# Kernel tuning notes

Measured on AMD Instinct MI355X. Metric: run time of the kernel, lower is better.

The kernel has to match this reference:

```python
import jax, jax.numpy as jnp
import numpy as np

N_NODES = 100000


def _gcn_conv(x, W, b, src, dst, ew, num_nodes):
    # PyG GCNConv: symmetric normalization with self-loops already included
    # in (src, dst, ew). deg computed on destination (col) index.
    deg = jax.ops.segment_sum(ew, dst, num_segments=num_nodes)  # [N]
    dinv = jnp.where(deg > 0, jax.lax.rsqrt(deg), 0.0)          # [N]
    norm = dinv[src] * ew * dinv[dst]                           # [E]
    h = x @ W                                                   # [N, out]
    msg = h[src] * norm[:, None]                                # [E, out] gather+scale
    out = jax.ops.segment_sum(msg, dst, num_segments=num_nodes) # scatter-add
    return out + b


def setup_inputs() -> dict:
    key = jax.random.key(0)
    k = jax.random.split(key, 8)
    in_c, hid_c, out_c = 128, 128, 64
    E, EL = 1600000, 200000
    x = jax.random.normal(k[0], (N_NODES, in_c), dtype=jnp.float32)
    edge_index = jax.random.randint(k[1], (2, E), 0, N_NODES, dtype=jnp.int64)
    edge_weight = jax.random.uniform(k[2], (E,), dtype=jnp.float32)
    edge_label_index = jax.random.randint(k[3], (2, EL), 0, N_NODES, dtype=jnp.int64)
    # Glorot-ish params
    W1 = jax.random.normal(k[4], (in_c, hid_c), dtype=jnp.float32) / np.sqrt(in_c)
    b1 = jnp.zeros((hid_c,), dtype=jnp.float32)
    W2 = jax.random.normal(k[5], (hid_c, out_c), dtype=jnp.float32) / np.sqrt(hid_c)
    b2 = jnp.zeros((out_c,), dtype=jnp.float32)
    return {"x": x, "edge_index": edge_index, "edge_weight": edge_weight,
            "edge_label_index": edge_label_index,
            "W1": W1, "b1": b1, "W2": W2, "b2": b2}


def reference(x, edge_index, edge_weight, edge_label_index, W1, b1, W2, b2):
    n = x.shape[0]
    # add self-loops (weight 1.0), static shape
    loop = jnp.arange(n, dtype=edge_index.dtype)
    src = jnp.concatenate([edge_index[0], loop])
    dst = jnp.concatenate([edge_index[1], loop])
    ew = jnp.concatenate([edge_weight, jnp.ones((n,), dtype=edge_weight.dtype)])
    h = jax.nn.relu(_gcn_conv(x, W1, b1, src, dst, ew, n))
    z = _gcn_conv(h, W2, b2, src, dst, ew, n)          # [N, out_c]
    # decode: edge dot-product
    return (z[edge_label_index[0]] * z[edge_label_index[1]]).sum(axis=-1)
```

## Files before the change

kernel.cpp:

```cpp
#include <hip/hip_runtime.h>
#include <math.h>

__global__ __launch_bounds__(256) void gemm128_hist_kernel(
        const float* __restrict__ X, const float* __restrict__ W, float* __restrict__ Y, int n,
        const int* __restrict__ dst, int* __restrict__ cnt, int* __restrict__ rank, int E) {
    constexpr int CG  = 32;
    constexpr int RG  = 8;
    constexpr int M   = 64;
    constexpr int RT  = 8;
    constexpr int KC  = 32;
    constexpr int LDX = 132;
    __shared__ float  Xl[M * LDX];
    __shared__ float4 Wl[KC * CG];

    const int bid = blockIdx.x;
    const int t = threadIdx.x;
    const int EPB = (E + (int)gridDim.x - 1) / (int)gridDim.x;
    const int eBeg = bid * EPB;
    const int eEnd = min(eBeg + EPB, E);

    if ((bid & 1) == 0) {
        for (int e = eBeg + t; e < eEnd; e += 256)
            rank[e] = atomicAdd(&cnt[dst[e]], 1);
    }

    int row0 = bid * M;
    {
        const float4* Xg = (const float4*)X;
        for (int f = t; f < M * 32; f += 256) {
            int r = f >> 5, c4 = f & 31;
            int gr = row0 + r;
            float4 v = make_float4(0.f, 0.f, 0.f, 0.f);
            if (gr < n) v = Xg[(size_t)gr * 32 + c4];
            *(float4*)&Xl[r * LDX + c4 * 4] = v;
        }
    }

    int cg = t % CG;
    int r0 = (t / CG) * RT;

    float4 acc[RT];
#pragma unroll
    for (int r = 0; r < RT; r++) acc[r] = make_float4(0.f, 0.f, 0.f, 0.f);

    const float4* Wg = (const float4*)W;
    for (int kc = 0; kc < 128; kc += KC) {
        __syncthreads();
        for (int f = t; f < KC * CG; f += 256)
            Wl[f] = Wg[(size_t)kc * CG + f];
        __syncthreads();
#pragma unroll 4
        for (int k = 0; k < KC; k += 4) {
            float4 b0 = Wl[(k + 0) * CG + cg];
            float4 b1 = Wl[(k + 1) * CG + cg];
            float4 b2 = Wl[(k + 2) * CG + cg];
            float4 b3 = Wl[(k + 3) * CG + cg];
#pragma unroll
            for (int r = 0; r < RT; r++) {
                float4 a = *(float4*)&Xl[(r0 + r) * LDX + kc + k];
                acc[r].x += a.x * b0.x + a.y * b1.x + a.z * b2.x + a.w * b3.x;
                acc[r].y += a.x * b0.y + a.y * b1.y + a.z * b2.y + a.w * b3.y;
                acc[r].z += a.x * b0.z + a.y * b1.z + a.z * b2.z + a.w * b3.z;
                acc[r].w += a.x * b0.w + a.y * b1.w + a.z * b2.w + a.w * b3.w;
            }
        }
    }

#pragma unroll
    for (int r = 0; r < RT; r++) {
        int gr = row0 + r0 + r;
        if (gr < n) *(float4*)&Y[(size_t)gr * 128 + cg * 4] = acc[r];
    }

    if (bid & 1) {
        for (int e = eBeg + t; e < eEnd; e += 256)
            rank[e] = atomicAdd(&cnt[dst[e]], 1);
    }
}

__global__ __launch_bounds__(256) void scan_block(const int* __restrict__ in, int* __restrict__ out,
                                                  int* __restrict__ bsum, int n) {
    __shared__ int s[256];
    int tid = threadIdx.x;
    int base = blockIdx.x * 1024 + tid * 4;
    int a0 = (base + 0 < n) ? in[base + 0] : 0;
    int a1 = (base + 1 < n) ? in[base + 1] : 0;
    int a2 = (base + 2 < n) ? in[base + 2] : 0;
    int a3 = (base + 3 < n) ? in[base + 3] : 0;
    int tsum = a0 + a1 + a2 + a3;
    s[tid] = tsum;
    __syncthreads();
    for (int off = 1; off < 256; off <<= 1) {
        int v = (tid >= off) ? s[tid - off] : 0;
        __syncthreads();
        s[tid] += v;
        __syncthreads();
    }
    int texcl = s[tid] - tsum;
    if (base + 0 < n) out[base + 0] = texcl;
    if (base + 1 < n) out[base + 1] = texcl + a0;
    if (base + 2 < n) out[base + 2] = texcl + a0 + a1;
    if (base + 3 < n) out[base + 3] = texcl + a0 + a1 + a2;
    if (tid == 255) bsum[blockIdx.x] = s[255];
}

__global__ __launch_bounds__(256) void scan_bsums(int* __restrict__ bsum, int nb) {
    __shared__ int s[256];
    __shared__ int carry_s;
    int tid = threadIdx.x;
    if (tid == 0) carry_s = 0;
    __syncthreads();
    for (int base = 0; base < nb; base += 256) {
        int v = (base + tid < nb) ? bsum[base + tid] : 0;
        int orig = v;
        s[tid] = v;
        __syncthreads();
        for (int off = 1; off < 256; off <<= 1) {
            int u = (tid >= off) ? s[tid - off] : 0;
            __syncthreads();
            s[tid] += u;
            __syncthreads();
        }
        int carry = carry_s;
        int excl = s[tid] - orig + carry;
        if (base + tid < nb) bsum[base + tid] = excl;
        int tot = s[255];
        __syncthreads();
        if (tid == 0) carry_s = carry + tot;
        __syncthreads();
    }
}

__global__ void scan_add(int* __restrict__ rowptr, const int* __restrict__ bscan, int n) {
    int t = blockIdx.x * blockDim.x + threadIdx.x;
    if (t < n) rowptr[t] += bscan[t >> 10];
}

__global__ void scatter_pairs(const int* __restrict__ src, const int* __restrict__ dst,
                              const float* __restrict__ ew, const int* __restrict__ rowptr,
                              const int* __restrict__ rank, int2* __restrict__ pairs, int E) {
    int e = blockIdx.x * blockDim.x + threadIdx.x;
    if (e >= E) return;
    int d = dst[e];
    int p = rowptr[d] + rank[e];
    pairs[p] = make_int2(src[e], __float_as_int(ew[e]));
}

__global__ void deg_dinv_kernel(const int2* __restrict__ pairs, const int* __restrict__ rowptr,
                                float* __restrict__ dinv, int n) {
    int i = blockIdx.x * blockDim.x + threadIdx.x;
    if (i >= n) return;
    int beg = rowptr[i], end = rowptr[i + 1];
    float s = 0.f;
    for (int j = beg; j < end; j++) s += __int_as_float(pairs[j].y);
    dinv[i] = 1.0f / sqrtf(s + 1.0f);
}

__global__ void norm_kernel(int2* __restrict__ pairs, const float* __restrict__ dinv, int E) {
    int j = blockIdx.x * blockDim.x + threadIdx.x;
    if (j >= E) return;
    int2 pr = pairs[j];
    pairs[j].y = __float_as_int(__int_as_float(pr.y) * dinv[pr.x]);
}

__global__ __launch_bounds__(256) void gather_mv_kernel(const float* __restrict__ H,
                                                        const int* __restrict__ rowptr,
                                                        const int2* __restrict__ pairs,
                                                        const float* __restrict__ dinv,
                                                        const float* __restrict__ bias,
                                                        const float* __restrict__ W2,
                                                        float* __restrict__ Z, int n) {
    __shared__ float h1s[8 * 128];
    __shared__ float w2s[32 * 64];
    const int t = threadIdx.x;
    const int nl = t >> 5;
    const int c4 = t & 31;
    const int node = blockIdx.x * 8 + nl;
    const float4* H4 = (const float4*)H;

    float4 a0 = make_float4(0.f, 0.f, 0.f, 0.f);
    float di = 0.f;
    if (node < n) {
        int beg = rowptr[node], end = rowptr[node + 1];
        di = dinv[node];
        float4 hv = H4[(size_t)node * 32 + c4];
        a0.x = hv.x * di; a0.y = hv.y * di; a0.z = hv.z * di; a0.w = hv.w * di;
        float4 a1 = make_float4(0.f, 0.f, 0.f, 0.f);
        float4 a2 = make_float4(0.f, 0.f, 0.f, 0.f);
        float4 a3 = make_float4(0.f, 0.f, 0.f, 0.f);
        int j = beg;
        for (; j + 8 <= end; j += 8) {
            int2 p0 = pairs[j + 0], p1 = pairs[j + 1], p2 = pairs[j + 2], p3 = pairs[j + 3];
            int2 p4 = pairs[j + 4], p5 = pairs[j + 5], p6 = pairs[j + 6], p7 = pairs[j + 7];
            float4 v0 = H4[(size_t)p0.x * 32 + c4];
            float4 v1 = H4[(size_t)p1.x * 32 + c4];
            float4 v2 = H4[(size_t)p2.x * 32 + c4];
            float4 v3 = H4[(size_t)p3.x * 32 + c4];
            float4 v4 = H4[(size_t)p4.x * 32 + c4];
            float4 v5 = H4[(size_t)p5.x * 32 + c4];
            float4 v6 = H4[(size_t)p6.x * 32 + c4];
            float4 v7 = H4[(size_t)p7.x * 32 + c4];
            float w0 = __int_as_float(p0.y), w1 = __int_as_float(p1.y);
            float w2 = __int_as_float(p2.y), w3 = __int_as_float(p3.y);
            float w4 = __int_as_float(p4.y), w5 = __int_as_float(p5.y);
            float w6 = __int_as_float(p6.y), w7 = __int_as_float(p7.y);
            a0.x += v0.x * w0; a0.y += v0.y * w0; a0.z += v0.z * w0; a0.w += v0.w * w0;
            a1.x += v1.x * w1; a1.y += v1.y * w1; a1.z += v1.z * w1; a1.w += v1.w * w1;
            a2.x += v2.x * w2; a2.y += v2.y * w2; a2.z += v2.z * w2; a2.w += v2.w * w2;
            a3.x += v3.x * w3; a3.y += v3.y * w3; a3.z += v3.z * w3; a3.w += v3.w * w3;
            a0.x += v4.x * w4; a0.y += v4.y * w4; a0.z += v4.z * w4; a0.w += v4.w * w4;
            a1.x += v5.x * w5; a1.y += v5.y * w5; a1.z += v5.z * w5; a1.w += v5.w * w5;
            a2.x += v6.x * w6; a2.y += v6.y * w6; a2.z += v6.z * w6; a2.w += v6.w * w6;
            a3.x += v7.x * w7; a3.y += v7.y * w7; a3.z += v7.z * w7; a3.w += v7.w * w7;
        }
        if (j + 4 <= end) {
            int2 p0 = pairs[j + 0], p1 = pairs[j + 1], p2 = pairs[j + 2], p3 = pairs[j + 3];
            float4 v0 = H4[(size_t)p0.x * 32 + c4];
            float4 v1 = H4[(size_t)p1.x * 32 + c4];
            float4 v2 = H4[(size_t)p2.x * 32 + c4];
            float4 v3 = H4[(size_t)p3.x * 32 + c4];
            float w0 = __int_as_float(p0.y), w1 = __int_as_float(p1.y);
            float w2 = __int_as_float(p2.y), w3 = __int_as_float(p3.y);
            a0.x += v0.x * w0; a0.y += v0.y * w0; a0.z += v0.z * w0; a0.w += v0.w * w0;
            a1.x += v1.x * w1; a1.y += v1.y * w1; a1.z += v1.z * w1; a1.w += v1.w * w1;
            a2.x += v2.x * w2; a2.y += v2.y * w2; a2.z += v2.z * w2; a2.w += v2.w * w2;
            a3.x += v3.x * w3; a3.y += v3.y * w3; a3.z += v3.z * w3; a3.w += v3.w * w3;
            j += 4;
        }
        for (; j < end; j++) {
            int2 pr = pairs[j];
            float w = __int_as_float(pr.y);
            float4 v = H4[(size_t)pr.x * 32 + c4];
            a0.x += v.x * w; a0.y += v.y * w; a0.z += v.z * w; a0.w += v.w * w;
        }
        float4 bb = ((const float4*)bias)[c4];
        a0.x = fmaxf(((a0.x + a1.x) + (a2.x + a3.x)) * di + bb.x, 0.f);
        a0.y = fmaxf(((a0.y + a1.y) + (a2.y + a3.y)) * di + bb.y, 0.f);
        a0.z = fmaxf(((a0.z + a1.z) + (a2.z + a3.z)) * di + bb.z, 0.f);
        a0.w = fmaxf(((a0.w + a1.w) + (a2.w + a3.w)) * di + bb.w, 0.f);
    }
    *(float4*)&h1s[nl * 128 + c4 * 4] = a0;

    float z0 = 0.f, z1 = 0.f;
    for (int kc = 0; kc < 128; kc += 32) {
        __syncthreads();
        {
            const float4* W2g = (const float4*)(W2 + kc * 64);
            float4* w2s4 = (float4*)w2s;
            for (int f = t; f < 512; f += 256) w2s4[f] = W2g[f];
        }
        __syncthreads();
        const float* hrow = &h1s[nl * 128 + kc];
        const float2* w2c = (const float2*)w2s;
#pragma unroll 8
        for (int k = 0; k < 32; k++) {
            float hk = hrow[k];
            float2 w = w2c[k * 32 + c4];
            z0 += hk * w.x;
            z1 += hk * w.y;
        }
    }
    if (node < n) *(float2*)&Z[(size_t)node * 64 + c4 * 2] = make_float2(z0, z1);
}

template<int C, bool RELU>
__global__ __launch_bounds__(256) void gather_reduce(const float* __restrict__ H,
                                                     const int* __restrict__ rowptr,
                                                     const int2* __restrict__ pairs,
                                                     const float* __restrict__ dinv,
                                                     const float* __restrict__ bias,
                                                     float* __restrict__ out, int n) {
    constexpr int TPN = C / 4;
    int t = blockIdx.x * blockDim.x + threadIdx.x;
    int node = t / TPN;
    int c4 = t % TPN;
    if (node >= n) return;
    const float4* H4 = (const float4*)H;
    int beg = rowptr[node], end = rowptr[node + 1];
    float di = dinv[node];
    float4 hv = H4[(size_t)node * TPN + c4];
    float4 bb = ((const float4*)bias)[c4];
    float4 a0, a1, a2, a3;
    a0.x = hv.x * di; a0.y = hv.y * di; a0.z = hv.z * di; a0.w = hv.w * di;
    a1 = make_float4(0.f, 0.f, 0.f, 0.f);
    a2 = make_float4(0.f, 0.f, 0.f, 0.f);
    a3 = make_float4(0.f, 0.f, 0.f, 0.f);
    int j = beg;
    for (; j + 8 <= end; j += 8) {
        int2 p0 = pairs[j + 0], p1 = pairs[j + 1], p2 = pairs[j + 2], p3 = pairs[j + 3];
        int2 p4 = pairs[j + 4], p5 = pairs[j + 5], p6 = pairs[j + 6], p7 = pairs[j + 7];
        float4 v0 = H4[(size_t)p0.x * TPN + c4];
        float4 v1 = H4[(size_t)p1.x * TPN + c4];
        float4 v2 = H4[(size_t)p2.x * TPN + c4];
        float4 v3 = H4[(size_t)p3.x * TPN + c4];
        float4 v4 = H4[(size_t)p4.x * TPN + c4];
        float4 v5 = H4[(size_t)p5.x * TPN + c4];
        float4 v6 = H4[(size_t)p6.x * TPN + c4];
        float4 v7 = H4[(size_t)p7.x * TPN + c4];
        float w0 = __int_as_float(p0.y), w1 = __int_as_float(p1.y);
        float w2 = __int_as_float(p2.y), w3 = __int_as_float(p3.y);
        float w4 = __int_as_float(p4.y), w5 = __int_as_float(p5.y);
        float w6 = __int_as_float(p6.y), w7 = __int_as_float(p7.y);
        a0.x += v0.x * w0; a0.y += v0.y * w0; a0.z += v0.z * w0; a0.w += v0.w * w0;
        a1.x += v1.x * w1; a1.y += v1.y * w1; a1.z += v1.z * w1; a1.w += v1.w * w1;
        a2.x += v2.x * w2; a2.y += v2.y * w2; a2.z += v2.z * w2; a2.w += v2.w * w2;
        a3.x += v3.x * w3; a3.y += v3.y * w3; a3.z += v3.z * w3; a3.w += v3.w * w3;
        a0.x += v4.x * w4; a0.y += v4.y * w4; a0.z += v4.z * w4; a0.w += v4.w * w4;
        a1.x += v5.x * w5; a1.y += v5.y * w5; a1.z += v5.z * w5; a1.w += v5.w * w5;
        a2.x += v6.x * w6; a2.y += v6.y * w6; a2.z += v6.z * w6; a2.w += v6.w * w6;
        a3.x += v7.x * w7; a3.y += v7.y * w7; a3.z += v7.z * w7; a3.w += v7.w * w7;
    }
    if (j + 4 <= end) {
        int2 p0 = pairs[j + 0], p1 = pairs[j + 1], p2 = pairs[j + 2], p3 = pairs[j + 3];
        float4 v0 = H4[(size_t)p0.x * TPN + c4];
        float4 v1 = H4[(size_t)p1.x * TPN + c4];
        float4 v2 = H4[(size_t)p2.x * TPN + c4];
        float4 v3 = H4[(size_t)p3.x * TPN + c4];
        float w0 = __int_as_float(p0.y), w1 = __int_as_float(p1.y);
        float w2 = __int_as_float(p2.y), w3 = __int_as_float(p3.y);
        a0.x += v0.x * w0; a0.y += v0.y * w0; a0.z += v0.z * w0; a0.w += v0.w * w0;
        a1.x += v1.x * w1; a1.y += v1.y * w1; a1.z += v1.z * w1; a1.w += v1.w * w1;
        a2.x += v2.x * w2; a2.y += v2.y * w2; a2.z += v2.z * w2; a2.w += v2.w * w2;
        a3.x += v3.x * w3; a3.y += v3.y * w3; a3.z += v3.z * w3; a3.w += v3.w * w3;
        j += 4;
    }
    for (; j < end; j++) {
        int2 pr = pairs[j];
        float w = __int_as_float(pr.y);
        float4 v = H4[(size_t)pr.x * TPN + c4];
        a0.x += v.x * w; a0.y += v.y * w; a0.z += v.z * w; a0.w += v.w * w;
    }
    float4 acc;
    acc.x = ((a0.x + a1.x) + (a2.x + a3.x)) * di + bb.x;
    acc.y = ((a0.y + a1.y) + (a2.y + a3.y)) * di + bb.y;
    acc.z = ((a0.z + a1.z) + (a2.z + a3.z)) * di + bb.z;
    acc.w = ((a0.w + a1.w) + (a2.w + a3.w)) * di + bb.w;
    if (RELU) {
        acc.x = fmaxf(acc.x, 0.f);
        acc.y = fmaxf(acc.y, 0.f);
        acc.z = fmaxf(acc.z, 0.f);
        acc.w = fmaxf(acc.w, 0.f);
    }
    *(float4*)&out[(size_t)node * C + c4 * 4] = acc;
}

__global__ void decode_kernel(const float* __restrict__ Z, const int* __restrict__ ea,
                              const int* __restrict__ eb, float* __restrict__ out, int L) {
    int t = blockIdx.x * blockDim.x + threadIdx.x;
    int e = t >> 4;
    int c = (t & 15) << 2;
    if (e >= L) return;
    float4 za = *(const float4*)&Z[(size_t)ea[e] * 64 + c];
    float4 zb = *(const float4*)&Z[(size_t)eb[e] * 64 + c];
    float p = za.x * zb.x + za.y * zb.y + za.z * zb.z + za.w * zb.w;
    p += __shfl_xor(p, 1);
    p += __shfl_xor(p, 2);
    p += __shfl_xor(p, 4);
    p += __shfl_xor(p, 8);
    if ((t & 15) == 0) out[e] = p;
}

extern "C" void kernel_launch(void* const* d_in, const int* in_sizes, int n_in,
                              void* d_out, int out_size, void* d_ws, size_t ws_size,
                              hipStream_t stream) {
    const float* x   = (const float*)d_in[0];
    const int*   ei  = (const int*)d_in[1];
    const float* ew  = (const float*)d_in[2];
    const int*   eli = (const int*)d_in[3];
    const float* W1  = (const float*)d_in[4];
    const float* b1  = (const float*)d_in[5];
    const float* W2  = (const float*)d_in[6];
    const float* b2  = (const float*)d_in[7];
    float* out = (float*)d_out;

    const int N = in_sizes[0] / 128;
    const int E = in_sizes[2];
    const int L = in_sizes[3] / 2;
    const int NP = ((N + 255) / 256) * 256;

    float* ws     = (float*)d_ws;
    float* dinv   = ws;
    int*   cnt    = (int*)(ws + NP);
    int*   rowptr = cnt + NP;
    int*   bsum   = rowptr + NP;
    int*   rank   = bsum + 1024;
    int2*  pairs  = (int2*)(rank + E);
    float* A      = (float*)(pairs + E);
    float* B      = A + (size_t)NP * 128;

    const int n1 = N + 1;
    const int nb = (n1 + 1023) / 1024;

    hipMemsetAsync(cnt, 0, (size_t)n1 * 4, stream);

    const int Gg = (N + 63) / 64;
    gemm128_hist_kernel<<<Gg, 256, 0, stream>>>(x, W1, A, N, ei + E, cnt, rank, E);

    scan_block<<<nb, 256, 0, stream>>>(cnt, rowptr, bsum, n1);
    scan_bsums<<<1, 256, 0, stream>>>(bsum, nb);
    scan_add<<<(n1 + 255) / 256, 256, 0, stream>>>(rowptr, bsum, n1);
    scatter_pairs<<<(E + 255) / 256, 256, 0, stream>>>(ei, ei + E, ew, rowptr, rank, pairs, E);
    deg_dinv_kernel<<<(N + 255) / 256, 256, 0, stream>>>(pairs, rowptr, dinv, N);
    norm_kernel<<<(E + 255) / 256, 256, 0, stream>>>(pairs, dinv, E);

    gather_mv_kernel<<<(N + 7) / 8, 256, 0, stream>>>(A, rowptr, pairs, dinv, b1, W2, B, N);

    gather_reduce<64, false><<<(N * 16 + 255) / 256, 256, 0, stream>>>(B, rowptr, pairs, dinv, b2, A, N);

    decode_kernel<<<(L * 16 + 255) / 256, 256, 0, stream>>>(A, eli, eli + L, out, L);
}
```

Baseline: 491.9 us.

## Fold source-side normalization into gather kernels and stage full W2 in LDS once

```diff
diff --git a/kernel.cpp b/kernel.cpp
--- a/kernel.cpp
+++ b/kernel.cpp
@@ -156,13 +156,6 @@
     dinv[i] = 1.0f / sqrtf(s + 1.0f);
 }
 
-__global__ void norm_kernel(int2* __restrict__ pairs, const float* __restrict__ dinv, int E) {
-    int j = blockIdx.x * blockDim.x + threadIdx.x;
-    if (j >= E) return;
-    int2 pr = pairs[j];
-    pairs[j].y = __float_as_int(__int_as_float(pr.y) * dinv[pr.x]);
-}
-
 __global__ __launch_bounds__(256) void gather_mv_kernel(const float* __restrict__ H,
                                                         const int* __restrict__ rowptr,
                                                         const int2* __restrict__ pairs,
@@ -171,18 +164,24 @@
                                                         const float* __restrict__ W2,
                                                         float* __restrict__ Z, int n) {
     __shared__ float h1s[8 * 128];
-    __shared__ float w2s[32 * 64];
+    __shared__ float w2s[128 * 64];
     const int t = threadIdx.x;
     const int nl = t >> 5;
     const int c4 = t & 31;
     const int node = blockIdx.x * 8 + nl;
     const float4* H4 = (const float4*)H;
 
+    {
+        const float4* W2g = (const float4*)W2;
+        float4* w2s4 = (float4*)w2s;
+#pragma unroll
+        for (int f = 0; f < 8; f++) w2s4[f * 256 + t] = W2g[f * 256 + t];
+    }
+
     float4 a0 = make_float4(0.f, 0.f, 0.f, 0.f);
-    float di = 0.f;
     if (node < n) {
         int beg = rowptr[node], end = rowptr[node + 1];
-        di = dinv[node];
+        float di = dinv[node];
         float4 hv = H4[(size_t)node * 32 + c4];
         a0.x = hv.x * di; a0.y = hv.y * di; a0.z = hv.z * di; a0.w = hv.w * di;
         float4 a1 = make_float4(0.f, 0.f, 0.f, 0.f);
@@ -200,10 +199,14 @@
             float4 v5 = H4[(size_t)p5.x * 32 + c4];
             float4 v6 = H4[(size_t)p6.x * 32 + c4];
             float4 v7 = H4[(size_t)p7.x * 32 + c4];
-            float w0 = __int_as_float(p0.y), w1 = __int_as_float(p1.y);
-            float w2 = __int_as_float(p2.y), w3 = __int_as_float(p3.y);
-            float w4 = __int_as_float(p4.y), w5 = __int_as_float(p5.y);
-            float w6 = __int_as_float(p6.y), w7 = __int_as_float(p7.y);
+            float w0 = dinv[p0.x] * __int_as_float(p0.y);
+            float w1 = dinv[p1.x] * __int_as_float(p1.y);
+            float w2 = dinv[p2.x] * __int_as_float(p2.y);
+            float w3 = dinv[p3.x] * __int_as_float(p3.y);
+            float w4 = dinv[p4.x] * __int_as_float(p4.y);
+            float w5 = dinv[p5.x] * __int_as_float(p5.y);
+            float w6 = dinv[p6.x] * __int_as_float(p6.y);
+            float w7 = dinv[p7.x] * __int_as_float(p7.y);
             a0.x += v0.x * w0; a0.y += v0.y * w0; a0.z += v0.z * w0; a0.w += v0.w * w0;
             a1.x += v1.x * w1; a1.y += v1.y * w1; a1.z += v1.z * w1; a1.w += v1.w * w1;
             a2.x += v2.x * w2; a2.y += v2.y * w2; a2.z += v2.z * w2; a2.w += v2.w * w2;
@@ -219,8 +222,10 @@
             float4 v1 = H4[(size_t)p1.x * 32 + c4];
             float4 v2 = H4[(size_t)p2.x * 32 + c4];
             float4 v3 = H4[(size_t)p3.x * 32 + c4];
-            float w0 = __int_as_float(p0.y), w1 = __int_as_float(p1.y);
-            float w2 = __int_as_float(p2.y), w3 = __int_as_float(p3.y);
+            float w0 = dinv[p0.x] * __int_as_float(p0.y);
+            float w1 = dinv[p1.x] * __int_as_float(p1.y);
+            float w2 = dinv[p2.x] * __int_as_float(p2.y);
+            float w3 = dinv[p3.x] * __int_as_float(p3.y);
             a0.x += v0.x * w0; a0.y += v0.y * w0; a0.z += v0.z * w0; a0.w += v0.w * w0;
             a1.x += v1.x * w1; a1.y += v1.y * w1; a1.z += v1.z * w1; a1.w += v1.w * w1;
             a2.x += v2.x * w2; a2.y += v2.y * w2; a2.z += v2.z * w2; a2.w += v2.w * w2;
@@ -229,7 +234,7 @@
         }
         for (; j < end; j++) {
             int2 pr = pairs[j];
-            float w = __int_as_float(pr.y);
+            float w = dinv[pr.x] * __int_as_float(pr.y);
             float4 v = H4[(size_t)pr.x * 32 + c4];
             a0.x += v.x * w; a0.y += v.y * w; a0.z += v.z * w; a0.w += v.w * w;
         }
@@ -240,25 +245,17 @@
         a0.w = fmaxf(((a0.w + a1.w) + (a2.w + a3.w)) * di + bb.w, 0.f);
     }
     *(float4*)&h1s[nl * 128 + c4 * 4] = a0;
+    __syncthreads();
 
     float z0 = 0.f, z1 = 0.f;
-    for (int kc = 0; kc < 128; kc += 32) {
-        __syncthreads();
-        {
-            const float4* W2g = (const float4*)(W2 + kc * 64);
-            float4* w2s4 = (float4*)w2s;
-            for (int f = t; f < 512; f += 256) w2s4[f] = W2g[f];
-        }
-        __syncthreads();
-        const float* hrow = &h1s[nl * 128 + kc];
-        const float2* w2c = (const float2*)w2s;
+    const float* hrow = &h1s[nl * 128];
+    const float2* w2c = (const float2*)w2s;
 #pragma unroll 8
-        for (int k = 0; k < 32; k++) {
-            float hk = hrow[k];
-            float2 w = w2c[k * 32 + c4];
-            z0 += hk * w.x;
-            z1 += hk * w.y;
-        }
+    for (int k = 0; k < 128; k++) {
+        float hk = hrow[k];
+        float2 w = w2c[k * 32 + c4];
+        z0 += hk * w.x;
+        z1 += hk * w.y;
     }
     if (node < n) *(float2*)&Z[(size_t)node * 64 + c4 * 2] = make_float2(z0, z1);
 }
@@ -297,10 +294,14 @@
         float4 v5 = H4[(size_t)p5.x * TPN + c4];
         float4 v6 = H4[(size_t)p6.x * TPN + c4];
         float4 v7 = H4[(size_t)p7.x * TPN + c4];
-        float w0 = __int_as_float(p0.y), w1 = __int_as_float(p1.y);
-        float w2 = __int_as_float(p2.y), w3 = __int_as_float(p3.y);
-        float w4 = __int_as_float(p4.y), w5 = __int_as_float(p5.y);
-        float w6 = __int_as_float(p6.y), w7 = __int_as_float(p7.y);
+        float w0 = dinv[p0.x] * __int_as_float(p0.y);
+        float w1 = dinv[p1.x] * __int_as_float(p1.y);
+        float w2 = dinv[p2.x] * __int_as_float(p2.y);
+        float w3 = dinv[p3.x] * __int_as_float(p3.y);
+        float w4 = dinv[p4.x] * __int_as_float(p4.y);
+        float w5 = dinv[p5.x] * __int_as_float(p5.y);
+        float w6 = dinv[p6.x] * __int_as_float(p6.y);
+        float w7 = dinv[p7.x] * __int_as_float(p7.y);
         a0.x += v0.x * w0; a0.y += v0.y * w0; a0.z += v0.z * w0; a0.w += v0.w * w0;
         a1.x += v1.x * w1; a1.y += v1.y * w1; a1.z += v1.z * w1; a1.w += v1.w * w1;
         a2.x += v2.x * w2; a2.y += v2.y * w2; a2.z += v2.z * w2; a2.w += v2.w * w2;
@@ -316,8 +317,10 @@
         float4 v1 = H4[(size_t)p1.x * TPN + c4];
         float4 v2 = H4[(size_t)p2.x * TPN + c4];
         float4 v3 = H4[(size_t)p3.x * TPN + c4];
-        float w0 = __int_as_float(p0.y), w1 = __int_as_float(p1.y);
-        float w2 = __int_as_float(p2.y), w3 = __int_as_float(p3.y);
+        float w0 = dinv[p0.x] * __int_as_float(p0.y);
+        float w1 = dinv[p1.x] * __int_as_float(p1.y);
+        float w2 = dinv[p2.x] * __int_as_float(p2.y);
+        float w3 = dinv[p3.x] * __int_as_float(p3.y);
         a0.x += v0.x * w0; a0.y += v0.y * w0; a0.z += v0.z * w0; a0.w += v0.w * w0;
         a1.x += v1.x * w1; a1.y += v1.y * w1; a1.z += v1.z * w1; a1.w += v1.w * w1;
         a2.x += v2.x * w2; a2.y += v2.y * w2; a2.z += v2.z * w2; a2.w += v2.w * w2;
@@ -326,7 +329,7 @@
     }
     for (; j < end; j++) {
         int2 pr = pairs[j];
-        float w = __int_as_float(pr.y);
+        float w = dinv[pr.x] * __int_as_float(pr.y);
         float4 v = H4[(size_t)pr.x * TPN + c4];
         a0.x += v.x * w; a0.y += v.y * w; a0.z += v.z * w; a0.w += v.w * w;
     }
@@ -401,7 +404,6 @@
     scan_add<<<(n1 + 255) / 256, 256, 0, stream>>>(rowptr, bsum, n1);
     scatter_pairs<<<(E + 255) / 256, 256, 0, stream>>>(ei, ei + E, ew, rowptr, rank, pairs, E);
     deg_dinv_kernel<<<(N + 255) / 256, 256, 0, stream>>>(pairs, rowptr, dinv, N);
-    norm_kernel<<<(E + 255) / 256, 256, 0, stream>>>(pairs, dinv, E);
 
     gather_mv_kernel<<<(N + 7) / 8, 256, 0, stream>>>(A, rowptr, pairs, dinv, b1, W2, B, N);
 
```

After: 484.2 us. Within noise of the previous version (-1.6%).
